# Kernel tuning notes

Hardware: AMD Instinct MI355X
Metric: run time of the kernel (lower is better)

## Reference

```python
import jax, jax.numpy as jnp
import numpy as np

EPSILON = 0.01
MAX_ITER = 100
CLAMP_MAX = 50.0
EPS_DIV = 1e-8


def setup_inputs() -> dict:
    key = jax.random.key(0)
    k1, k2 = jax.random.split(key)
    B, N, M = 8, 2048, 2048
    source = jax.random.normal(k1, (B, N, 3), dtype=jnp.float32)
    target = jax.random.normal(k2, (B, M, 3), dtype=jnp.float32)
    return {"source": source, "target": target}


def reference(source, target):
    # source: (B, N, 3), target: (B, M, 3)
    B, N, _ = source.shape
    M = target.shape[1]
    # Pairwise Euclidean cost matrix: (B, N, M)
    diff = source[:, :, None, :] - target[:, None, :, :]
    cost = jnp.linalg.norm(diff, axis=-1)
    # Entropic kernel with clamp to avoid underflow (matches torch.clamp(max=50))
    K = jnp.exp(-jnp.minimum(cost / EPSILON, CLAMP_MAX))
    mu = jnp.full((B, N), 1.0 / N, dtype=source.dtype)
    nu = jnp.full((B, M), 1.0 / M, dtype=source.dtype)
    u0 = jnp.ones_like(mu)
    v0 = jnp.ones_like(nu)

    def step(carry, _):
        u, v = carry
        Kv = jnp.einsum('bnm,bm->bn', K, v)
        u = mu / jnp.maximum(Kv, EPS_DIV)
        Ktu = jnp.einsum('bnm,bn->bm', K, u)
        v = nu / jnp.maximum(Ktu, EPS_DIV)
        return (u, v), None

    (u, v), _ = jax.lax.scan(step, (u0, v0), None, length=MAX_ITER)
    # Transport plan T = diag(u) K diag(v); emd = sum(T * cost)
    T = u[:, :, None] * K * v[:, None, :]
    emd = jnp.sum(T * cost, axis=(1, 2))  # (B,)
    return jnp.mean(emd)  # reduction='mean'
```

## Files before the change

kernel.cpp:

```cpp
#include <hip/hip_runtime.h>
#include <stdint.h>
#include <stddef.h>

#define BATCH 8
#define NPT   2048
#define NB    (BATCH*NPT)
#define CAP   128
#define ITERS 100
#define TPB   1024
#define NWAVE (TPB/64)
#define C50      1.9287498479639178e-22f
#define MUV      (1.0f/2048.0f)
#define EPS_DIVF 1e-8f
#define R2THR 0.1089f

#define OFF_GMAX 0u
#define OFF_CNT  4096u
#define OFF_PERM (OFF_CNT  + (size_t)2*NB*2)
#define OFF_IPRM (OFF_PERM + (size_t)2*NB*2)
#define OFF_SPTS (OFF_IPRM + (size_t)2*NB*2)
#define OFF_TPTS (OFF_SPTS + (size_t)NB*16)
#define OFF_U    (OFF_TPTS + (size_t)NB*16)
#define OFF_V    (OFF_U + (size_t)NB*4)
#define OFF_ROWE (OFF_V + (size_t)NB*4)
#define OFF_COLE (OFF_ROWE + (size_t)NB*CAP*4)

__device__ __forceinline__ uint32_t pack_entry(float kv, int idx) {
    return (__float_as_uint(kv) & 0xFFFFC000u) | ((uint32_t)idx << 2);
}

__device__ __forceinline__ uint32_t pi_map(uint32_t i) {
    return (i & 0x7E0u) | ((i ^ (i >> 5)) & 31u);
}

__device__ __forceinline__ size_t ellt4_addr(int ofs, int p) {
    return (size_t)(ofs >> 2) * (NPT*4) + (size_t)p * 4 + (ofs & 3);
}

extern "C" __global__ __launch_bounds__(TPB, 2)
void emd_count_56831007261025(const float* __restrict__ src,
                              const float* __restrict__ tgt,
                              uint8_t* __restrict__ wsb,
                              float* __restrict__ out)
{
    __shared__ float4 opts[NPT];

    uint16_t* cnt   = (uint16_t*)(wsb + OFF_CNT);
    float4*   gspts = (float4*)  (wsb + OFF_SPTS);
    float4*   gtpts = (float4*)  (wsb + OFF_TPTS);
    uint32_t* scr1  = (uint32_t*)(wsb + OFF_U);
    uint32_t* rowE  = (uint32_t*)(wsb + OFF_ROWE);
    uint32_t* colE  = (uint32_t*)(wsb + OFF_COLE);

    const int tid  = threadIdx.x;
    const int lane = tid & 63;
    const int wid  = tid >> 6;
    const int b    = blockIdx.x >> 5;
    const int g    = blockIdx.x & 31;
    const size_t base = (size_t)b * NPT;

    if (blockIdx.x == 0 && tid == 0) *out = 0.0f;

    if (tid < 64) {
        size_t gi = base + g*64 + tid;
        gspts[gi] = make_float4(src[3*gi], src[3*gi+1], src[3*gi+2], 0.0f);
        gtpts[gi] = make_float4(tgt[3*gi], tgt[3*gi+1], tgt[3*gi+2], 0.0f);
        scr1[(size_t)blockIdx.x*64 + tid] = 0u;
    }

    {
        const size_t ebase = (size_t)b * NPT * CAP;
        for (int idx = tid; idx < 32*256; idx += TPB) {
            int j4 = idx >> 8, t = idx & 255;
            size_t a = ebase + (size_t)j4*(NPT*4) + (size_t)g*256 + t;
            rowE[a] = 0u;
            colE[a] = 0u;
        }
    }

    for (int pass = 0; pass < 2; ++pass) {
        const float* mineRaw  = pass ? tgt : src;
        const float* cloudRaw = pass ? src : tgt;

        __syncthreads();
        for (int i = tid; i < NPT; i += TPB) {
            size_t gi = base + i;
            opts[i] = make_float4(cloudRaw[3*gi], cloudRaw[3*gi+1], cloudRaw[3*gi+2], 0.0f);
        }
        __syncthreads();

        for (int r = 0; r < 4; ++r) {
            int n = g*64 + wid*4 + r;
            size_t gi = base + n;
            float4 sp = make_float4(mineRaw[3*gi], mineRaw[3*gi+1], mineRaw[3*gi+2], 0.0f);
            uint32_t c = 0;
            for (int mb = 0; mb < NPT; mb += 64) {
                float4 tp = opts[mb + lane];
                float dx = sp.x - tp.x, dy = sp.y - tp.y, dz = sp.z - tp.z;
                float d2 = dx*dx + dy*dy + dz*dz;
                c += (uint32_t)__popcll(__ballot(d2 < R2THR));
            }
            if (lane == 0) cnt[(size_t)pass*NB + gi] = (uint16_t)((c < CAP) ? c : CAP);
        }
    }
}

extern "C" __global__ __launch_bounds__(256, 4)
void emd_sort_56831007261025(uint8_t* __restrict__ wsb)
{
    __shared__ uint32_t hist[CAP+2];
    __shared__ uint32_t bofs[CAP+2];
    __shared__ uint16_t permL[NPT];

    const int tid = threadIdx.x;
    const int dir = blockIdx.x >> 3;
    const int b   = blockIdx.x & 7;

    const uint16_t* cnt  = (const uint16_t*)(wsb + OFF_CNT) + (size_t)dir*NB + (size_t)b*NPT;
    uint16_t*       perm = (uint16_t*)(wsb + OFF_PERM) + (size_t)dir*NB + (size_t)b*NPT;
    uint16_t*       inv  = (uint16_t*)(wsb + OFF_IPRM) + (size_t)dir*NB + (size_t)b*NPT;
    uint32_t*       gmax = (uint32_t*)(wsb + OFF_GMAX) + (size_t)dir*256 + (size_t)b*32;

    for (int i = tid; i < CAP+2; i += 256) hist[i] = 0;
    __syncthreads();
    for (int n = tid; n < NPT; n += 256) atomicAdd(&hist[cnt[n]], 1u);
    __syncthreads();
    if (tid == 0) {
        uint32_t run = 0;
        for (int i = 0; i < CAP+2; ++i) { bofs[i] = run; run += hist[i]; }
    }
    __syncthreads();
    for (int n = tid; n < NPT; n += 256) {
        uint32_t p = atomicAdd(&bofs[cnt[n]], 1u);
        permL[p] = (uint16_t)n;
    }
    __syncthreads();
    for (int p = tid; p < NPT; p += 256) {
        uint16_t o = permL[p];
        perm[p] = o;
        inv[o]  = (uint16_t)p;
    }
    if (tid < 32) gmax[tid] = cnt[permL[tid*64 + 63]];
}

extern "C" __global__ __launch_bounds__(TPB, 2)
void emd_build_56831007261025(uint8_t* __restrict__ wsb)
{
    __shared__ float4   opts[NPT];
    __shared__ uint16_t rows[64];
    __shared__ uint16_t invp[NPT];

    const float4* gspts = (const float4*)(wsb + OFF_SPTS);
    const float4* gtpts = (const float4*)(wsb + OFF_TPTS);
    uint32_t*     rowE  = (uint32_t*)(wsb + OFF_ROWE);
    uint32_t*     colE  = (uint32_t*)(wsb + OFF_COLE);

    const int tid  = threadIdx.x;
    const int lane = tid & 63;
    const int wid  = tid >> 6;
    const int b    = blockIdx.x >> 5;
    const int g    = blockIdx.x & 31;
    const size_t base  = (size_t)b * NPT;
    const size_t ebase = (size_t)b * NPT * CAP;

    uint32_t* scr1 = (uint32_t*)(wsb + OFF_U) + base;
    const uint16_t* permG = (const uint16_t*)(wsb + OFF_PERM) + base;
    const uint16_t* invG  = (const uint16_t*)(wsb + OFF_IPRM) + (size_t)NB + base;

    for (int i = tid; i < NPT; i += TPB) {
        opts[i] = gtpts[base + i];
        invp[i] = invG[i];
    }
    if (tid < 64) rows[tid] = permG[g*64 + tid];
    __syncthreads();

    for (int r = 0; r < 4; ++r) {
        int psort = g*64 + wid*4 + r;
        int n     = rows[wid*4 + r];
        float4 sp = gspts[base + n];
        uint32_t c = 0;
        for (int mb = 0; mb < NPT; mb += 64) {
            int m = mb + lane;
            float4 tp = opts[m];
            float dx = sp.x - tp.x, dy = sp.y - tp.y, dz = sp.z - tp.z;
            float d2 = dx*dx + dy*dy + dz*dz;
            bool p = d2 < R2THR;
            uint64_t mask = __ballot(p);
            if (p) {
                float d  = sqrtf(d2);
                float kv = expf(-100.0f * d) - C50;
                uint32_t ofs = c + (uint32_t)__popcll(mask & ((1ull << lane) - 1ull));
                if (ofs < CAP)
                    rowE[ebase + ellt4_addr((int)ofs, psort)] = pack_entry(kv, invp[m]);
                uint32_t q  = invp[m];
                uint32_t oj = atomicAdd(&scr1[m], 1u);
                if (oj < CAP)
                    colE[ebase + ellt4_addr((int)oj, (int)q)] = pack_entry(kv, psort);
            }
            c += (uint32_t)__popcll(mask);
        }
    }
}

extern "C" __global__ __launch_bounds__(64)
void emd_sched_56831007261025(uint8_t* __restrict__ wsb)
{
    __shared__ uint32_t se[32*256];
    __shared__ uint8_t  cw[64*32];

    const int tid = threadIdx.x;
    const int blk = blockIdx.x;
    const int g   = blk & 31;
    const int b   = (blk >> 5) & 7;
    const int dir = blk >> 8;

    const size_t ebase = (size_t)b * NPT * CAP;
    uint32_t* E = (uint32_t*)(wsb + (dir ? OFF_COLE : OFF_ROWE)) + ebase;
    const uint32_t* gmax = (const uint32_t*)(wsb + OFF_GMAX) + (size_t)dir*256 + (size_t)b*32;

    const int cm4 = ((int)gmax[g] + 3) >> 2;
    const int S   = cm4 * 4;

    for (int j4 = 0; j4 < cm4; ++j4)
        *(uint4*)&se[j4*256 + tid*4] = *(const uint4*)(E + (size_t)j4*(NPT*4) + (size_t)g*256 + (size_t)tid*4);
    __syncthreads();

    for (int s0 = tid; s0 < S; s0 += 64) {
        *(uint64_t*)(cw + tid*32 +  0) = 0ull;
        *(uint64_t*)(cw + tid*32 +  8) = 0ull;
        *(uint64_t*)(cw + tid*32 + 16) = 0ull;
        *(uint64_t*)(cw + tid*32 + 24) = 0ull;

        const int base = (s0 >> 2)*256 + (s0 & 3);
        uint64_t padmask = 0ull;
        for (int t = 0; t < 64; ++t) {
            uint32_t e = se[base + t*4];
            if ((e >> 14) == 0u) { padmask |= 1ull << t; continue; }
            uint32_t i  = (e >> 2) & 0x7FFu;
            uint32_t p1 = pi_map(i);
            uint32_t b0 = i & 31u, b1 = p1 & 31u;
            uint8_t  c0 = cw[tid*32 + b0], c1 = cw[tid*32 + b1];
            uint32_t idx;
            if (c1 < c0) { idx = 2048u + p1; cw[tid*32 + b1] = (uint8_t)(c1 + 1); }
            else         { idx = i;          cw[tid*32 + b0] = (uint8_t)(c0 + 1); }
            se[base + t*4] = (e & 0xFFFFC000u) | (idx << 2);
        }
        if (padmask) {
            uint32_t best = 0, bc = 255;
            for (uint32_t bb = 0; bb < 32; ++bb) {
                uint32_t c = cw[tid*32 + bb];
                if (c < bc) { bc = c; best = bb; }
            }
            uint32_t pw = (2048u + best) << 2;
            while (padmask) {
                int t = __ffsll((unsigned long long)padmask) - 1;
                padmask &= padmask - 1;
                se[base + t*4] = pw;
            }
        }
    }
    __syncthreads();

    for (int j4 = 0; j4 < cm4; ++j4)
        *(uint4*)(E + (size_t)j4*(NPT*4) + (size_t)g*256 + (size_t)tid*4) = *(const uint4*)&se[j4*256 + tid*4];
}

__device__ __forceinline__ uint4 ldE(const uint32_t* ep, int j4) {
    return *(const uint4*)(ep + (size_t)j4 * (NPT*4));
}

#define GATHER(e, OFS) (*(const float*)((const uint8_t*)W + (OFS) + ((e) & 0x3FFCu)))
#define FMA4C(a0, a1, a2, a3, e4, OFS) do { \
    a0 = fmaf(__uint_as_float((e4).x), GATHER((e4).x, OFS), a0); \
    a1 = fmaf(__uint_as_float((e4).y), GATHER((e4).y, OFS), a1); \
    a2 = fmaf(__uint_as_float((e4).z), GATHER((e4).z, OFS), a2); \
    a3 = fmaf(__uint_as_float((e4).w), GATHER((e4).w, OFS), a3); \
} while (0)

#define SCAN(OFS) do { \
    FMA4C(A0,A1,A2,A3, pfA0, OFS); FMA4C(A0,A1,A2,A3, pfA1, OFS); \
    FMA4C(B0,B1,B2,B3, pfB0, OFS); FMA4C(B0,B1,B2,B3, pfB1, OFS); \
    int j4 = 2; \
    for (; j4 + 1 < jmin; j4 += 2) { \
        uint4 x0 = ldE(eA, j4),   y0 = ldE(eB, j4); \
        uint4 x1 = ldE(eA, j4+1), y1 = ldE(eB, j4+1); \
        FMA4C(A0,A1,A2,A3, x0, OFS); FMA4C(B0,B1,B2,B3, y0, OFS); \
        FMA4C(A0,A1,A2,A3, x1, OFS); FMA4C(B0,B1,B2,B3, y1, OFS); \
    } \
    if (j4 < jmin) { \
        uint4 x0 = ldE(eA, j4), y0 = ldE(eB, j4); \
        FMA4C(A0,A1,A2,A3, x0, OFS); FMA4C(B0,B1,B2,B3, y0, OFS); \
        ++j4; \
    } \
    for (; j4 + 1 < jbig; j4 += 2) { \
        uint4 x0 = ldE(eL, j4), x1 = ldE(eL, j4+1); \
        FMA4C(R0,R1,R2,R3, x0, OFS); FMA4C(R4,R5,R6,R7, x1, OFS); \
    } \
    if (j4 < jbig) { uint4 x0 = ldE(eL, j4); FMA4C(R0,R1,R2,R3, x0, OFS); } \
} while (0)

extern "C" __global__ __launch_bounds__(TPB, 1)
void emd_iterate_56831007261025(uint8_t* __restrict__ wsb,
                                float* __restrict__ out)
{
    __shared__ float    W[8192];
    __shared__ float4   red[2][NWAVE/4];
    __shared__ uint32_t gmL[2][32];

    const int tid  = threadIdx.x;
    const int lane = tid & 63;
    const int wid  = tid >> 6;
    const int b    = blockIdx.x;
    const size_t ebase = (size_t)b * NPT * CAP;

    const uint32_t* rowE = (const uint32_t*)(wsb + OFF_ROWE) + ebase;
    const uint32_t* colE = (const uint32_t*)(wsb + OFF_COLE) + ebase;
    const uint32_t* gmax = (const uint32_t*)(wsb + OFF_GMAX);

    if (tid < 32) {
        gmL[0][tid] = gmax[(size_t)b*32 + tid];
        gmL[1][tid] = gmax[256 + (size_t)b*32 + tid];
    }
    for (int i = tid; i < 4096; i += TPB) W[4096 + i] = 1.0f;
    __syncthreads();

    const int gA = wid, gB = 31 - wid;
    const int posA = gA*64 + lane, posB = gB*64 + lane;
    const int pA1 = 2048 + (int)pi_map((uint32_t)posA);
    const int pB1 = 2048 + (int)pi_map((uint32_t)posB);
    const int jAu = (__builtin_amdgcn_readfirstlane((int)gmL[0][gA]) + 3) >> 2;
    const int jBu = (__builtin_amdgcn_readfirstlane((int)gmL[0][gB]) + 3) >> 2;
    const int jAv = (__builtin_amdgcn_readfirstlane((int)gmL[1][gA]) + 3) >> 2;
    const int jBv = (__builtin_amdgcn_readfirstlane((int)gmL[1][gB]) + 3) >> 2;
    const uint32_t* rA = rowE + (size_t)posA * 4;
    const uint32_t* rB = rowE + (size_t)posB * 4;
    const uint32_t* cA = colE + (size_t)posA * 4;
    const uint32_t* cB = colE + (size_t)posB * 4;

    uint4 pfA0 = ldE(rA, 0), pfA1 = ldE(rA, 1);
    uint4 pfB0 = ldE(rB, 0), pfB1 = ldE(rB, 1);

    for (int ph = 0; ph < 2*ITERS; ++ph) {
        const bool up = (ph & 1) == 0;
        const int jA = up ? jAu : jAv;
        const int jB = up ? jBu : jBv;
        const uint32_t* eA = up ? rA : cA;
        const uint32_t* eB = up ? rB : cB;
        const uint32_t* eL = (jA > jB) ? eA : eB;
        const int jmin = (jA < jB) ? jA : jB;
        const int jbig = (jA > jB) ? jA : jB;

        float A0=0.f,A1=0.f,A2=0.f,A3=0.f, B0=0.f,B1=0.f,B2=0.f,B3=0.f;
        float R0=0.f,R1=0.f,R2=0.f,R3=0.f, R4=0.f,R5=0.f,R6=0.f,R7=0.f;

        if (up) SCAN(16384); else SCAN(0);

        float accA = (A0+A1)+(A2+A3);
        float accB = (B0+B1)+(B2+B3);
        float accR = ((R0+R1)+(R2+R3)) + ((R4+R5)+(R6+R7));
        if (jA > jB) accA += accR; else accB += accR;

        const uint32_t* nA = up ? cA : rA;
        const uint32_t* nB = up ? cB : rB;
        pfA0 = ldE(nA, 0); pfA1 = ldE(nA, 1);
        pfB0 = ldE(nB, 0); pfB1 = ldE(nB, 1);

        float Sw;
        if (ph == 0) {
            Sw = (float)NPT;
        } else {
            const float4* rp = red[(ph - 1) & 1];
            float4 r0 = rp[0], r1 = rp[1], r2 = rp[2], r3 = rp[3];
            Sw = (((r0.x+r0.y)+(r0.z+r0.w)) + ((r1.x+r1.y)+(r1.z+r1.w)))
               + (((r2.x+r2.y)+(r2.z+r2.w)) + ((r3.x+r3.y)+(r3.z+r3.w)));
        }

        const int wrofs = up ? 0 : 4096;
        float valA = MUV * __builtin_amdgcn_rcpf(fmaxf(fmaf(C50, Sw, accA), EPS_DIVF));
        float valB = MUV * __builtin_amdgcn_rcpf(fmaxf(fmaf(C50, Sw, accB), EPS_DIVF));
        W[wrofs + posA] = valA;   W[wrofs + pA1] = valA;
        W[wrofs + posB] = valB;   W[wrofs + pB1] = valB;

        float psum = valA + valB;
        #pragma unroll
        for (int o = 32; o > 0; o >>= 1) psum += __shfl_down(psum, o, 64);
        if (lane == 0) ((float*)red[ph & 1])[wid] = psum;

        __syncthreads();
    }

    {
        float accA = 0.0f, accB = 0.0f;
        for (int pr = 0; pr < 2; ++pr) {
            const uint32_t* ep = pr ? rB : rA;
            const int jm = pr ? jBu : jAu;
            float a0 = 0.0f, a1 = 0.0f;
            for (int j4 = 0; j4 < jm; ++j4) {
                uint4 e4 = ldE(ep, j4);
                uint32_t ee[4] = { e4.x, e4.y, e4.z, e4.w };
                #pragma unroll
                for (int k = 0; k < 4; ++k) {
                    uint32_t e = ee[k];
                    if ((e >> 14) != 0u) {
                        float kv = __uint_as_float(e & 0xFFFFC000u);
                        float d  = -0.01f * logf(kv);
                        float t  = kv * GATHER(e, 16384);
                        if (k & 1) a1 = fmaf(t, d, a1); else a0 = fmaf(t, d, a0);
                    }
                }
            }
            if (pr) accB = a0 + a1; else accA = a0 + a1;
        }
        float psum = W[posA] * accA + W[posB] * accB;
        #pragma unroll
        for (int o = 32; o > 0; o >>= 1) psum += __shfl_down(psum, o, 64);
        if (lane == 0) ((float*)red[0])[wid] = psum;
        __syncthreads();
        if (tid == 0) {
            const float* rp = (const float*)red[0];
            float t = 0.0f;
            #pragma unroll
            for (int w = 0; w < NWAVE; ++w) t += rp[w];
            atomicAdd(out, t * 0.125f);
        }
    }
}

extern "C" void kernel_launch(void* const* d_in, const int* in_sizes, int n_in,
                              void* d_out, int out_size, void* d_ws, size_t ws_size,
                              hipStream_t stream)
{
    const float* src = (const float*)d_in[0];
    const float* tgt = (const float*)d_in[1];
    float* out = (float*)d_out;
    uint8_t* ws = (uint8_t*)d_ws;

    emd_count_56831007261025  <<<dim3(256), dim3(TPB), 0, stream>>>(src, tgt, ws, out);
    emd_sort_56831007261025   <<<dim3(16),  dim3(256), 0, stream>>>(ws);
    emd_build_56831007261025  <<<dim3(256), dim3(TPB), 0, stream>>>(ws);
    emd_sched_56831007261025  <<<dim3(512), dim3(64),  0, stream>>>(ws);
    emd_iterate_56831007261025<<<dim3(8),   dim3(TPB), 0, stream>>>(ws, out);
}
```

Baseline: 458.5 us.

## Fuse all five stages into one cooperative kernel with grid syncs

Replaces the count, sort, build, schedule and iterate kernels with one cooperative-launched kernel that separates the stages with grid.sync() and shares one union of LDS buffers. The column counts are now gathered with global atomics during the first pass, so the second counting pass over the mirrored direction is gone. The schedule stage now uses 1024-thread blocks instead of 64-thread ones. The goal is to remove four kernel launch gaps and one redundant distance pass. In exchange, every stage runs at the grid size of 256 large blocks, adds atomic contention, and the final 200-phase iteration still uses only 8 blocks.

```diff
diff --git a/kernel.cpp b/kernel.cpp
--- a/kernel.cpp
+++ b/kernel.cpp
@@ -1,6 +1,9 @@
 #include <hip/hip_runtime.h>
+#include <hip/hip_cooperative_groups.h>
 #include <stdint.h>
 #include <stddef.h>
+
+namespace cg = cooperative_groups;
 
 #define BATCH 8
 #define NPT   2048
@@ -35,234 +38,6 @@
 
 __device__ __forceinline__ size_t ellt4_addr(int ofs, int p) {
     return (size_t)(ofs >> 2) * (NPT*4) + (size_t)p * 4 + (ofs & 3);
-}
-
-extern "C" __global__ __launch_bounds__(TPB, 2)
-void emd_count_56831007261025(const float* __restrict__ src,
-                              const float* __restrict__ tgt,
-                              uint8_t* __restrict__ wsb,
-                              float* __restrict__ out)
-{
-    __shared__ float4 opts[NPT];
-
-    uint16_t* cnt   = (uint16_t*)(wsb + OFF_CNT);
-    float4*   gspts = (float4*)  (wsb + OFF_SPTS);
-    float4*   gtpts = (float4*)  (wsb + OFF_TPTS);
-    uint32_t* scr1  = (uint32_t*)(wsb + OFF_U);
-    uint32_t* rowE  = (uint32_t*)(wsb + OFF_ROWE);
-    uint32_t* colE  = (uint32_t*)(wsb + OFF_COLE);
-
-    const int tid  = threadIdx.x;
-    const int lane = tid & 63;
-    const int wid  = tid >> 6;
-    const int b    = blockIdx.x >> 5;
-    const int g    = blockIdx.x & 31;
-    const size_t base = (size_t)b * NPT;
-
-    if (blockIdx.x == 0 && tid == 0) *out = 0.0f;
-
-    if (tid < 64) {
-        size_t gi = base + g*64 + tid;
-        gspts[gi] = make_float4(src[3*gi], src[3*gi+1], src[3*gi+2], 0.0f);
-        gtpts[gi] = make_float4(tgt[3*gi], tgt[3*gi+1], tgt[3*gi+2], 0.0f);
-        scr1[(size_t)blockIdx.x*64 + tid] = 0u;
-    }
-
-    {
-        const size_t ebase = (size_t)b * NPT * CAP;
-        for (int idx = tid; idx < 32*256; idx += TPB) {
-            int j4 = idx >> 8, t = idx & 255;
-            size_t a = ebase + (size_t)j4*(NPT*4) + (size_t)g*256 + t;
-            rowE[a] = 0u;
-            colE[a] = 0u;
-        }
-    }
-
-    for (int pass = 0; pass < 2; ++pass) {
-        const float* mineRaw  = pass ? tgt : src;
-        const float* cloudRaw = pass ? src : tgt;
-
-        __syncthreads();
-        for (int i = tid; i < NPT; i += TPB) {
-            size_t gi = base + i;
-            opts[i] = make_float4(cloudRaw[3*gi], cloudRaw[3*gi+1], cloudRaw[3*gi+2], 0.0f);
-        }
-        __syncthreads();
-
-        for (int r = 0; r < 4; ++r) {
-            int n = g*64 + wid*4 + r;
-            size_t gi = base + n;
-            float4 sp = make_float4(mineRaw[3*gi], mineRaw[3*gi+1], mineRaw[3*gi+2], 0.0f);
-            uint32_t c = 0;
-            for (int mb = 0; mb < NPT; mb += 64) {
-                float4 tp = opts[mb + lane];
-                float dx = sp.x - tp.x, dy = sp.y - tp.y, dz = sp.z - tp.z;
-                float d2 = dx*dx + dy*dy + dz*dz;
-                c += (uint32_t)__popcll(__ballot(d2 < R2THR));
-            }
-            if (lane == 0) cnt[(size_t)pass*NB + gi] = (uint16_t)((c < CAP) ? c : CAP);
-        }
-    }
-}
-
-extern "C" __global__ __launch_bounds__(256, 4)
-void emd_sort_56831007261025(uint8_t* __restrict__ wsb)
-{
-    __shared__ uint32_t hist[CAP+2];
-    __shared__ uint32_t bofs[CAP+2];
-    __shared__ uint16_t permL[NPT];
-
-    const int tid = threadIdx.x;
-    const int dir = blockIdx.x >> 3;
-    const int b   = blockIdx.x & 7;
-
-    const uint16_t* cnt  = (const uint16_t*)(wsb + OFF_CNT) + (size_t)dir*NB + (size_t)b*NPT;
-    uint16_t*       perm = (uint16_t*)(wsb + OFF_PERM) + (size_t)dir*NB + (size_t)b*NPT;
-    uint16_t*       inv  = (uint16_t*)(wsb + OFF_IPRM) + (size_t)dir*NB + (size_t)b*NPT;
-    uint32_t*       gmax = (uint32_t*)(wsb + OFF_GMAX) + (size_t)dir*256 + (size_t)b*32;
-
-    for (int i = tid; i < CAP+2; i += 256) hist[i] = 0;
-    __syncthreads();
-    for (int n = tid; n < NPT; n += 256) atomicAdd(&hist[cnt[n]], 1u);
-    __syncthreads();
-    if (tid == 0) {
-        uint32_t run = 0;
-        for (int i = 0; i < CAP+2; ++i) { bofs[i] = run; run += hist[i]; }
-    }
-    __syncthreads();
-    for (int n = tid; n < NPT; n += 256) {
-        uint32_t p = atomicAdd(&bofs[cnt[n]], 1u);
-        permL[p] = (uint16_t)n;
-    }
-    __syncthreads();
-    for (int p = tid; p < NPT; p += 256) {
-        uint16_t o = permL[p];
-        perm[p] = o;
-        inv[o]  = (uint16_t)p;
-    }
-    if (tid < 32) gmax[tid] = cnt[permL[tid*64 + 63]];
-}
-
-extern "C" __global__ __launch_bounds__(TPB, 2)
-void emd_build_56831007261025(uint8_t* __restrict__ wsb)
-{
-    __shared__ float4   opts[NPT];
-    __shared__ uint16_t rows[64];
-    __shared__ uint16_t invp[NPT];
-
-    const float4* gspts = (const float4*)(wsb + OFF_SPTS);
-    const float4* gtpts = (const float4*)(wsb + OFF_TPTS);
-    uint32_t*     rowE  = (uint32_t*)(wsb + OFF_ROWE);
-    uint32_t*     colE  = (uint32_t*)(wsb + OFF_COLE);
-
-    const int tid  = threadIdx.x;
-    const int lane = tid & 63;
-    const int wid  = tid >> 6;
-    const int b    = blockIdx.x >> 5;
-    const int g    = blockIdx.x & 31;
-    const size_t base  = (size_t)b * NPT;
-    const size_t ebase = (size_t)b * NPT * CAP;
-
-    uint32_t* scr1 = (uint32_t*)(wsb + OFF_U) + base;
-    const uint16_t* permG = (const uint16_t*)(wsb + OFF_PERM) + base;
-    const uint16_t* invG  = (const uint16_t*)(wsb + OFF_IPRM) + (size_t)NB + base;
-
-    for (int i = tid; i < NPT; i += TPB) {
-        opts[i] = gtpts[base + i];
-        invp[i] = invG[i];
-    }
-    if (tid < 64) rows[tid] = permG[g*64 + tid];
-    __syncthreads();
-
-    for (int r = 0; r < 4; ++r) {
-        int psort = g*64 + wid*4 + r;
-        int n     = rows[wid*4 + r];
-        float4 sp = gspts[base + n];
-        uint32_t c = 0;
-        for (int mb = 0; mb < NPT; mb += 64) {
-            int m = mb + lane;
-            float4 tp = opts[m];
-            float dx = sp.x - tp.x, dy = sp.y - tp.y, dz = sp.z - tp.z;
-            float d2 = dx*dx + dy*dy + dz*dz;
-            bool p = d2 < R2THR;
-            uint64_t mask = __ballot(p);
-            if (p) {
-                float d  = sqrtf(d2);
-                float kv = expf(-100.0f * d) - C50;
-                uint32_t ofs = c + (uint32_t)__popcll(mask & ((1ull << lane) - 1ull));
-                if (ofs < CAP)
-                    rowE[ebase + ellt4_addr((int)ofs, psort)] = pack_entry(kv, invp[m]);
-                uint32_t q  = invp[m];
-                uint32_t oj = atomicAdd(&scr1[m], 1u);
-                if (oj < CAP)
-                    colE[ebase + ellt4_addr((int)oj, (int)q)] = pack_entry(kv, psort);
-            }
-            c += (uint32_t)__popcll(mask);
-        }
-    }
-}
-
-extern "C" __global__ __launch_bounds__(64)
-void emd_sched_56831007261025(uint8_t* __restrict__ wsb)
-{
-    __shared__ uint32_t se[32*256];
-    __shared__ uint8_t  cw[64*32];
-
-    const int tid = threadIdx.x;
-    const int blk = blockIdx.x;
-    const int g   = blk & 31;
-    const int b   = (blk >> 5) & 7;
-    const int dir = blk >> 8;
-
-    const size_t ebase = (size_t)b * NPT * CAP;
-    uint32_t* E = (uint32_t*)(wsb + (dir ? OFF_COLE : OFF_ROWE)) + ebase;
-    const uint32_t* gmax = (const uint32_t*)(wsb + OFF_GMAX) + (size_t)dir*256 + (size_t)b*32;
-
-    const int cm4 = ((int)gmax[g] + 3) >> 2;
-    const int S   = cm4 * 4;
-
-    for (int j4 = 0; j4 < cm4; ++j4)
-        *(uint4*)&se[j4*256 + tid*4] = *(const uint4*)(E + (size_t)j4*(NPT*4) + (size_t)g*256 + (size_t)tid*4);
-    __syncthreads();
-
-    for (int s0 = tid; s0 < S; s0 += 64) {
-        *(uint64_t*)(cw + tid*32 +  0) = 0ull;
-        *(uint64_t*)(cw + tid*32 +  8) = 0ull;
-        *(uint64_t*)(cw + tid*32 + 16) = 0ull;
-        *(uint64_t*)(cw + tid*32 + 24) = 0ull;
-
-        const int base = (s0 >> 2)*256 + (s0 & 3);
-        uint64_t padmask = 0ull;
-        for (int t = 0; t < 64; ++t) {
-            uint32_t e = se[base + t*4];
-            if ((e >> 14) == 0u) { padmask |= 1ull << t; continue; }
-            uint32_t i  = (e >> 2) & 0x7FFu;
-            uint32_t p1 = pi_map(i);
-            uint32_t b0 = i & 31u, b1 = p1 & 31u;
-            uint8_t  c0 = cw[tid*32 + b0], c1 = cw[tid*32 + b1];
-            uint32_t idx;
-            if (c1 < c0) { idx = 2048u + p1; cw[tid*32 + b1] = (uint8_t)(c1 + 1); }
-            else         { idx = i;          cw[tid*32 + b0] = (uint8_t)(c0 + 1); }
-            se[base + t*4] = (e & 0xFFFFC000u) | (idx << 2);
-        }
-        if (padmask) {
-            uint32_t best = 0, bc = 255;
-            for (uint32_t bb = 0; bb < 32; ++bb) {
-                uint32_t c = cw[tid*32 + bb];
-                if (c < bc) { bc = c; best = bb; }
-            }
-            uint32_t pw = (2048u + best) << 2;
-            while (padmask) {
-                int t = __ffsll((unsigned long long)padmask) - 1;
-                padmask &= padmask - 1;
-                se[base + t*4] = pw;
-            }
-        }
-    }
-    __syncthreads();
-
-    for (int j4 = 0; j4 < cm4; ++j4)
-        *(uint4*)(E + (size_t)j4*(NPT*4) + (size_t)g*256 + (size_t)tid*4) = *(const uint4*)&se[j4*256 + tid*4];
 }
 
 __device__ __forceinline__ uint4 ldE(const uint32_t* ep, int j4) {
@@ -299,129 +74,347 @@
     if (j4 < jbig) { uint4 x0 = ldE(eL, j4); FMA4C(R0,R1,R2,R3, x0, OFS); } \
 } while (0)
 
+union ShMem {
+    struct { float4 opts[NPT]; uint16_t rows[64]; uint16_t invp[NPT]; } bc;
+    struct { uint32_t hist[CAP+2]; uint32_t bofs[CAP+2]; uint16_t permL[NPT]; } s;
+    struct { uint32_t se[32*256]; uint8_t cw[128*32]; } f;
+    struct { float W[8192]; float4 red[2][NWAVE/4]; uint32_t gmL[2][32]; } d;
+};
+
 extern "C" __global__ __launch_bounds__(TPB, 1)
-void emd_iterate_56831007261025(uint8_t* __restrict__ wsb,
-                                float* __restrict__ out)
+void emd_fused_56831007261025(const float* __restrict__ src,
+                              const float* __restrict__ tgt,
+                              uint8_t* __restrict__ wsb,
+                              float* __restrict__ out)
 {
-    __shared__ float    W[8192];
-    __shared__ float4   red[2][NWAVE/4];
-    __shared__ uint32_t gmL[2][32];
+    __shared__ ShMem sh;
+    cg::grid_group grid = cg::this_grid();
 
     const int tid  = threadIdx.x;
     const int lane = tid & 63;
     const int wid  = tid >> 6;
-    const int b    = blockIdx.x;
-    const size_t ebase = (size_t)b * NPT * CAP;
-
-    const uint32_t* rowE = (const uint32_t*)(wsb + OFF_ROWE) + ebase;
-    const uint32_t* colE = (const uint32_t*)(wsb + OFF_COLE) + ebase;
-    const uint32_t* gmax = (const uint32_t*)(wsb + OFF_GMAX);
-
-    if (tid < 32) {
-        gmL[0][tid] = gmax[(size_t)b*32 + tid];
-        gmL[1][tid] = gmax[256 + (size_t)b*32 + tid];
-    }
-    for (int i = tid; i < 4096; i += TPB) W[4096 + i] = 1.0f;
-    __syncthreads();
-
-    const int gA = wid, gB = 31 - wid;
-    const int posA = gA*64 + lane, posB = gB*64 + lane;
-    const int pA1 = 2048 + (int)pi_map((uint32_t)posA);
-    const int pB1 = 2048 + (int)pi_map((uint32_t)posB);
-    const int jAu = (__builtin_amdgcn_readfirstlane((int)gmL[0][gA]) + 3) >> 2;
-    const int jBu = (__builtin_amdgcn_readfirstlane((int)gmL[0][gB]) + 3) >> 2;
-    const int jAv = (__builtin_amdgcn_readfirstlane((int)gmL[1][gA]) + 3) >> 2;
-    const int jBv = (__builtin_amdgcn_readfirstlane((int)gmL[1][gB]) + 3) >> 2;
-    const uint32_t* rA = rowE + (size_t)posA * 4;
-    const uint32_t* rB = rowE + (size_t)posB * 4;
-    const uint32_t* cA = colE + (size_t)posA * 4;
-    const uint32_t* cB = colE + (size_t)posB * 4;
-
-    uint4 pfA0 = ldE(rA, 0), pfA1 = ldE(rA, 1);
-    uint4 pfB0 = ldE(rB, 0), pfB1 = ldE(rB, 1);
-
-    for (int ph = 0; ph < 2*ITERS; ++ph) {
-        const bool up = (ph & 1) == 0;
-        const int jA = up ? jAu : jAv;
-        const int jB = up ? jBu : jBv;
-        const uint32_t* eA = up ? rA : cA;
-        const uint32_t* eB = up ? rB : cB;
-        const uint32_t* eL = (jA > jB) ? eA : eB;
-        const int jmin = (jA < jB) ? jA : jB;
-        const int jbig = (jA > jB) ? jA : jB;
-
-        float A0=0.f,A1=0.f,A2=0.f,A3=0.f, B0=0.f,B1=0.f,B2=0.f,B3=0.f;
-        float R0=0.f,R1=0.f,R2=0.f,R3=0.f, R4=0.f,R5=0.f,R6=0.f,R7=0.f;
-
-        if (up) SCAN(16384); else SCAN(0);
-
-        float accA = (A0+A1)+(A2+A3);
-        float accB = (B0+B1)+(B2+B3);
-        float accR = ((R0+R1)+(R2+R3)) + ((R4+R5)+(R6+R7));
-        if (jA > jB) accA += accR; else accB += accR;
-
-        const uint32_t* nA = up ? cA : rA;
-        const uint32_t* nB = up ? cB : rB;
-        pfA0 = ldE(nA, 0); pfA1 = ldE(nA, 1);
-        pfB0 = ldE(nB, 0); pfB1 = ldE(nB, 1);
-
-        float Sw;
-        if (ph == 0) {
-            Sw = (float)NPT;
-        } else {
-            const float4* rp = red[(ph - 1) & 1];
-            float4 r0 = rp[0], r1 = rp[1], r2 = rp[2], r3 = rp[3];
-            Sw = (((r0.x+r0.y)+(r0.z+r0.w)) + ((r1.x+r1.y)+(r1.z+r1.w)))
-               + (((r2.x+r2.y)+(r2.z+r2.w)) + ((r3.x+r3.y)+(r3.z+r3.w)));
-        }
-
-        const int wrofs = up ? 0 : 4096;
-        float valA = MUV * __builtin_amdgcn_rcpf(fmaxf(fmaf(C50, Sw, accA), EPS_DIVF));
-        float valB = MUV * __builtin_amdgcn_rcpf(fmaxf(fmaf(C50, Sw, accB), EPS_DIVF));
-        W[wrofs + posA] = valA;   W[wrofs + pA1] = valA;
-        W[wrofs + posB] = valB;   W[wrofs + pB1] = valB;
-
-        float psum = valA + valB;
-        #pragma unroll
-        for (int o = 32; o > 0; o >>= 1) psum += __shfl_down(psum, o, 64);
-        if (lane == 0) ((float*)red[ph & 1])[wid] = psum;
-
-        __syncthreads();
-    }
+    const int bid  = blockIdx.x;
+
+    uint16_t* cnt0g = (uint16_t*)(wsb + OFF_CNT);
+    uint32_t* cnt1g = (uint32_t*)(wsb + OFF_V);
+    uint32_t* scr1g = (uint32_t*)(wsb + OFF_U);
+    float4*   gspts = (float4*)  (wsb + OFF_SPTS);
+    float4*   gtpts = (float4*)  (wsb + OFF_TPTS);
+    uint32_t* rowEg = (uint32_t*)(wsb + OFF_ROWE);
+    uint32_t* colEg = (uint32_t*)(wsb + OFF_COLE);
+    uint32_t* gmaxg = (uint32_t*)(wsb + OFF_GMAX);
+
+    if (bid == 0 && tid == 0) *out = 0.0f;
+    if (tid < 64) {
+        cnt1g[(size_t)bid*64 + tid] = 0u;
+        scr1g[(size_t)bid*64 + tid] = 0u;
+    }
+    grid.sync();
 
     {
-        float accA = 0.0f, accB = 0.0f;
-        for (int pr = 0; pr < 2; ++pr) {
-            const uint32_t* ep = pr ? rB : rA;
-            const int jm = pr ? jBu : jAu;
-            float a0 = 0.0f, a1 = 0.0f;
-            for (int j4 = 0; j4 < jm; ++j4) {
-                uint4 e4 = ldE(ep, j4);
-                uint32_t ee[4] = { e4.x, e4.y, e4.z, e4.w };
-                #pragma unroll
-                for (int k = 0; k < 4; ++k) {
-                    uint32_t e = ee[k];
-                    if ((e >> 14) != 0u) {
-                        float kv = __uint_as_float(e & 0xFFFFC000u);
-                        float d  = -0.01f * logf(kv);
-                        float t  = kv * GATHER(e, 16384);
-                        if (k & 1) a1 = fmaf(t, d, a1); else a0 = fmaf(t, d, a0);
+        const int b = bid >> 5, g = bid & 31;
+        const size_t base  = (size_t)b * NPT;
+        const size_t ebase = (size_t)b * NPT * CAP;
+
+        if (tid < 64) {
+            size_t gi = base + g*64 + tid;
+            gspts[gi] = make_float4(src[3*gi], src[3*gi+1], src[3*gi+2], 0.0f);
+            gtpts[gi] = make_float4(tgt[3*gi], tgt[3*gi+1], tgt[3*gi+2], 0.0f);
+        }
+        for (int idx = tid; idx < 32*256; idx += TPB) {
+            int j4 = idx >> 8, t = idx & 255;
+            size_t a = ebase + (size_t)j4*(NPT*4) + (size_t)g*256 + t;
+            rowEg[a] = 0u;
+            colEg[a] = 0u;
+        }
+        for (int i = tid; i < NPT; i += TPB) {
+            size_t gi = base + i;
+            sh.bc.opts[i] = make_float4(tgt[3*gi], tgt[3*gi+1], tgt[3*gi+2], 0.0f);
+        }
+        __syncthreads();
+
+        for (int r = 0; r < 4; ++r) {
+            int n = g*64 + wid*4 + r;
+            size_t gi = base + n;
+            float4 sp = make_float4(src[3*gi], src[3*gi+1], src[3*gi+2], 0.0f);
+            uint32_t c = 0;
+            for (int mb = 0; mb < NPT; mb += 64) {
+                int m = mb + lane;
+                float4 tp = sh.bc.opts[m];
+                float dx = sp.x - tp.x, dy = sp.y - tp.y, dz = sp.z - tp.z;
+                float d2 = dx*dx + dy*dy + dz*dz;
+                bool p = d2 < R2THR;
+                if (p) atomicAdd(&cnt1g[base + m], 1u);
+                c += (uint32_t)__popcll(__ballot(p));
+            }
+            if (lane == 0) cnt0g[gi] = (uint16_t)((c < CAP) ? c : CAP);
+        }
+    }
+    grid.sync();
+
+    if (bid < 16) {
+        const int dir = bid >> 3, b = bid & 7;
+        const size_t base = (size_t)b * NPT;
+        uint16_t* perm = (uint16_t*)(wsb + OFF_PERM) + (size_t)dir*NB + base;
+        uint16_t* inv  = (uint16_t*)(wsb + OFF_IPRM) + (size_t)dir*NB + base;
+        uint32_t* gmax = gmaxg + (size_t)dir*256 + (size_t)b*32;
+
+        for (int i = tid; i < CAP+2; i += TPB) sh.s.hist[i] = 0;
+        __syncthreads();
+        for (int n = tid; n < NPT; n += TPB) {
+            uint32_t cv = dir ? cnt1g[base + n] : (uint32_t)cnt0g[base + n];
+            if (cv > CAP) cv = CAP;
+            atomicAdd(&sh.s.hist[cv], 1u);
+        }
+        __syncthreads();
+        if (tid == 0) {
+            uint32_t run = 0;
+            for (int i = 0; i < CAP+2; ++i) { sh.s.bofs[i] = run; run += sh.s.hist[i]; }
+        }
+        __syncthreads();
+        for (int n = tid; n < NPT; n += TPB) {
+            uint32_t cv = dir ? cnt1g[base + n] : (uint32_t)cnt0g[base + n];
+            if (cv > CAP) cv = CAP;
+            uint32_t p = atomicAdd(&sh.s.bofs[cv], 1u);
+            sh.s.permL[p] = (uint16_t)n;
+        }
+        __syncthreads();
+        for (int p = tid; p < NPT; p += TPB) {
+            uint16_t o = sh.s.permL[p];
+            perm[p] = o;
+            inv[o]  = (uint16_t)p;
+        }
+        if (tid < 32) {
+            uint16_t o = sh.s.permL[tid*64 + 63];
+            uint32_t cv = dir ? cnt1g[base + o] : (uint32_t)cnt0g[base + o];
+            if (cv > CAP) cv = CAP;
+            gmax[tid] = cv;
+        }
+    }
+    grid.sync();
+
+    {
+        const int b = bid >> 5, g = bid & 31;
+        const size_t base  = (size_t)b * NPT;
+        const size_t ebase = (size_t)b * NPT * CAP;
+        uint32_t* scr1 = scr1g + base;
+        const uint16_t* permG = (const uint16_t*)(wsb + OFF_PERM) + base;
+        const uint16_t* invG  = (const uint16_t*)(wsb + OFF_IPRM) + (size_t)NB + base;
+
+        for (int i = tid; i < NPT; i += TPB) {
+            sh.bc.opts[i] = gtpts[base + i];
+            sh.bc.invp[i] = invG[i];
+        }
+        if (tid < 64) sh.bc.rows[tid] = permG[g*64 + tid];
+        __syncthreads();
+
+        for (int r = 0; r < 4; ++r) {
+            int psort = g*64 + wid*4 + r;
+            int n     = sh.bc.rows[wid*4 + r];
+            float4 sp = gspts[base + n];
+            uint32_t c = 0;
+            for (int mb = 0; mb < NPT; mb += 64) {
+                int m = mb + lane;
+                float4 tp = sh.bc.opts[m];
+                float dx = sp.x - tp.x, dy = sp.y - tp.y, dz = sp.z - tp.z;
+                float d2 = dx*dx + dy*dy + dz*dz;
+                bool p = d2 < R2THR;
+                uint64_t mask = __ballot(p);
+                if (p) {
+                    float d  = sqrtf(d2);
+                    float kv = expf(-100.0f * d) - C50;
+                    uint32_t ofs = c + (uint32_t)__popcll(mask & ((1ull << lane) - 1ull));
+                    if (ofs < CAP)
+                        rowEg[ebase + ellt4_addr((int)ofs, psort)] = pack_entry(kv, sh.bc.invp[m]);
+                    uint32_t q  = sh.bc.invp[m];
+                    uint32_t oj = atomicAdd(&scr1[m], 1u);
+                    if (oj < CAP)
+                        colEg[ebase + ellt4_addr((int)oj, (int)q)] = pack_entry(kv, psort);
+                }
+                c += (uint32_t)__popcll(mask);
+            }
+        }
+    }
+    grid.sync();
+
+    for (int tk = 0; tk < 2; ++tk) {
+        const int blk = bid*2 + tk;
+        const int g   = blk & 31;
+        const int b   = (blk >> 5) & 7;
+        const int dir = blk >> 8;
+        const size_t ebase = (size_t)b * NPT * CAP;
+        uint32_t* E = (dir ? colEg : rowEg) + ebase;
+        const uint32_t* gmax = gmaxg + (size_t)dir*256 + (size_t)b*32;
+
+        const int cm4 = ((int)gmax[g] + 3) >> 2;
+        const int S   = cm4 * 4;
+
+        __syncthreads();
+        for (int u = tid; u < cm4*64; u += TPB) {
+            int j4 = u >> 6, t = u & 63;
+            *(uint4*)&sh.f.se[j4*256 + t*4] =
+                *(const uint4*)(E + (size_t)j4*(NPT*4) + (size_t)g*256 + (size_t)t*4);
+        }
+        __syncthreads();
+
+        for (int s0 = tid; s0 < S; s0 += TPB) {
+            *(uint64_t*)(sh.f.cw + s0*32 +  0) = 0ull;
+            *(uint64_t*)(sh.f.cw + s0*32 +  8) = 0ull;
+            *(uint64_t*)(sh.f.cw + s0*32 + 16) = 0ull;
+            *(uint64_t*)(sh.f.cw + s0*32 + 24) = 0ull;
+
+            const int base = (s0 >> 2)*256 + (s0 & 3);
+            uint64_t padmask = 0ull;
+            for (int t = 0; t < 64; ++t) {
+                uint32_t e = sh.f.se[base + t*4];
+                if ((e >> 14) == 0u) { padmask |= 1ull << t; continue; }
+                uint32_t i  = (e >> 2) & 0x7FFu;
+                uint32_t p1 = pi_map(i);
+                uint32_t b0 = i & 31u, b1 = p1 & 31u;
+                uint8_t  c0 = sh.f.cw[s0*32 + b0], c1 = sh.f.cw[s0*32 + b1];
+                uint32_t idx;
+                if (c1 < c0) { idx = 2048u + p1; sh.f.cw[s0*32 + b1] = (uint8_t)(c1 + 1); }
+                else         { idx = i;          sh.f.cw[s0*32 + b0] = (uint8_t)(c0 + 1); }
+                sh.f.se[base + t*4] = (e & 0xFFFFC000u) | (idx << 2);
+            }
+            if (padmask) {
+                uint32_t best = 0, bc = 255;
+                for (uint32_t bb = 0; bb < 32; ++bb) {
+                    uint32_t c = sh.f.cw[s0*32 + bb];
+                    if (c < bc) { bc = c; best = bb; }
+                }
+                uint32_t pw = (2048u + best) << 2;
+                while (padmask) {
+                    int t = __ffsll((unsigned long long)padmask) - 1;
+                    padmask &= padmask - 1;
+                    sh.f.se[base + t*4] = pw;
+                }
+            }
+        }
+        __syncthreads();
+
+        for (int u = tid; u < cm4*64; u += TPB) {
+            int j4 = u >> 6, t = u & 63;
+            *(uint4*)(E + (size_t)j4*(NPT*4) + (size_t)g*256 + (size_t)t*4) =
+                *(const uint4*)&sh.f.se[j4*256 + t*4];
+        }
+    }
+    grid.sync();
+
+    if (bid >= BATCH) return;
+    {
+        const int b = bid;
+        const size_t ebase = (size_t)b * NPT * CAP;
+        const uint32_t* rowE = rowEg + ebase;
+        const uint32_t* colE = colEg + ebase;
+        float* const W = sh.d.W;
+
+        if (tid < 32) {
+            sh.d.gmL[0][tid] = gmaxg[(size_t)b*32 + tid];
+            sh.d.gmL[1][tid] = gmaxg[256 + (size_t)b*32 + tid];
+        }
+        for (int i = tid; i < 4096; i += TPB) W[4096 + i] = 1.0f;
+        __syncthreads();
+
+        const int gA = wid, gB = 31 - wid;
+        const int posA = gA*64 + lane, posB = gB*64 + lane;
+        const int pA1 = 2048 + (int)pi_map((uint32_t)posA);
+        const int pB1 = 2048 + (int)pi_map((uint32_t)posB);
+        const int jAu = (__builtin_amdgcn_readfirstlane((int)sh.d.gmL[0][gA]) + 3) >> 2;
+        const int jBu = (__builtin_amdgcn_readfirstlane((int)sh.d.gmL[0][gB]) + 3) >> 2;
+        const int jAv = (__builtin_amdgcn_readfirstlane((int)sh.d.gmL[1][gA]) + 3) >> 2;
+        const int jBv = (__builtin_amdgcn_readfirstlane((int)sh.d.gmL[1][gB]) + 3) >> 2;
+        const uint32_t* rA = rowE + (size_t)posA * 4;
+        const uint32_t* rB = rowE + (size_t)posB * 4;
+        const uint32_t* cA = colE + (size_t)posA * 4;
+        const uint32_t* cB = colE + (size_t)posB * 4;
+
+        uint4 pfA0 = ldE(rA, 0), pfA1 = ldE(rA, 1);
+        uint4 pfB0 = ldE(rB, 0), pfB1 = ldE(rB, 1);
+
+        for (int ph = 0; ph < 2*ITERS; ++ph) {
+            const bool up = (ph & 1) == 0;
+            const int jA = up ? jAu : jAv;
+            const int jB = up ? jBu : jBv;
+            const uint32_t* eA = up ? rA : cA;
+            const uint32_t* eB = up ? rB : cB;
+            const uint32_t* eL = (jA > jB) ? eA : eB;
+            const int jmin = (jA < jB) ? jA : jB;
+            const int jbig = (jA > jB) ? jA : jB;
+
+            float A0=0.f,A1=0.f,A2=0.f,A3=0.f, B0=0.f,B1=0.f,B2=0.f,B3=0.f;
+            float R0=0.f,R1=0.f,R2=0.f,R3=0.f, R4=0.f,R5=0.f,R6=0.f,R7=0.f;
+
+            if (up) SCAN(16384); else SCAN(0);
+
+            float accA = (A0+A1)+(A2+A3);
+            float accB = (B0+B1)+(B2+B3);
+            float accR = ((R0+R1)+(R2+R3)) + ((R4+R5)+(R6+R7));
+            if (jA > jB) accA += accR; else accB += accR;
+
+            const uint32_t* nA = up ? cA : rA;
+            const uint32_t* nB = up ? cB : rB;
+            pfA0 = ldE(nA, 0); pfA1 = ldE(nA, 1);
+            pfB0 = ldE(nB, 0); pfB1 = ldE(nB, 1);
+
+            float Sw;
+            if (ph == 0) {
+                Sw = (float)NPT;
+            } else {
+                const float4* rp = sh.d.red[(ph - 1) & 1];
+                float4 r0 = rp[0], r1 = rp[1], r2 = rp[2], r3 = rp[3];
+                Sw = (((r0.x+r0.y)+(r0.z+r0.w)) + ((r1.x+r1.y)+(r1.z+r1.w)))
+                   + (((r2.x+r2.y)+(r2.z+r2.w)) + ((r3.x+r3.y)+(r3.z+r3.w)));
+            }
+
+            const int wrofs = up ? 0 : 4096;
+            float valA = MUV * __builtin_amdgcn_rcpf(fmaxf(fmaf(C50, Sw, accA), EPS_DIVF));
+            float valB = MUV * __builtin_amdgcn_rcpf(fmaxf(fmaf(C50, Sw, accB), EPS_DIVF));
+            W[wrofs + posA] = valA;   W[wrofs + pA1] = valA;
+            W[wrofs + posB] = valB;   W[wrofs + pB1] = valB;
+
+            float psum = valA + valB;
+            #pragma unroll
+            for (int o = 32; o > 0; o >>= 1) psum += __shfl_down(psum, o, 64);
+            if (lane == 0) ((float*)sh.d.red[ph & 1])[wid] = psum;
+
+            __syncthreads();
+        }
+
+        {
+            float accA = 0.0f, accB = 0.0f;
+            for (int pr = 0; pr < 2; ++pr) {
+                const uint32_t* ep = pr ? rB : rA;
+                const int jm = pr ? jBu : jAu;
+                float a0 = 0.0f, a1 = 0.0f;
+                for (int j4 = 0; j4 < jm; ++j4) {
+                    uint4 e4 = ldE(ep, j4);
+                    uint32_t ee[4] = { e4.x, e4.y, e4.z, e4.w };
+                    #pragma unroll
+                    for (int k = 0; k < 4; ++k) {
+                        uint32_t e = ee[k];
+                        if ((e >> 14) != 0u) {
+                            float kv = __uint_as_float(e & 0xFFFFC000u);
+                            float d  = -0.01f * logf(kv);
+                            float t  = kv * GATHER(e, 16384);
+                            if (k & 1) a1 = fmaf(t, d, a1); else a0 = fmaf(t, d, a0);
+                        }
                     }
                 }
-            }
-            if (pr) accB = a0 + a1; else accA = a0 + a1;
-        }
-        float psum = W[posA] * accA + W[posB] * accB;
-        #pragma unroll
-        for (int o = 32; o > 0; o >>= 1) psum += __shfl_down(psum, o, 64);
-        if (lane == 0) ((float*)red[0])[wid] = psum;
-        __syncthreads();
-        if (tid == 0) {
-            const float* rp = (const float*)red[0];
-            float t = 0.0f;
+                if (pr) accB = a0 + a1; else accA = a0 + a1;
+            }
+            float psum = W[posA] * accA + W[posB] * accB;
             #pragma unroll
-            for (int w = 0; w < NWAVE; ++w) t += rp[w];
-            atomicAdd(out, t * 0.125f);
+            for (int o = 32; o > 0; o >>= 1) psum += __shfl_down(psum, o, 64);
+            if (lane == 0) ((float*)sh.d.red[0])[wid] = psum;
+            __syncthreads();
+            if (tid == 0) {
+                const float* rp = (const float*)sh.d.red[0];
+                float t = 0.0f;
+                #pragma unroll
+                for (int w = 0; w < NWAVE; ++w) t += rp[w];
+                atomicAdd(out, t * 0.125f);
+            }
         }
     }
 }
@@ -435,9 +428,7 @@
     float* out = (float*)d_out;
     uint8_t* ws = (uint8_t*)d_ws;
 
-    emd_count_56831007261025  <<<dim3(256), dim3(TPB), 0, stream>>>(src, tgt, ws, out);
-    emd_sort_56831007261025   <<<dim3(16),  dim3(256), 0, stream>>>(ws);
-    emd_build_56831007261025  <<<dim3(256), dim3(TPB), 0, stream>>>(ws);
-    emd_sched_56831007261025  <<<dim3(512), dim3(64),  0, stream>>>(ws);
-    emd_iterate_56831007261025<<<dim3(8),   dim3(TPB), 0, stream>>>(ws, out);
-}
+    void* args[] = { (void*)&src, (void*)&tgt, (void*)&ws, (void*)&out };
+    hipLaunchCooperativeKernel((const void*)emd_fused_56831007261025,
+                               dim3(256), dim3(TPB), args, 0, stream);
+}
```

Measured after the change: 628.9 us. 1.37x slower.
